# Kernel tuning notes

Measured on AMD Instinct MI355X. Metric: run time of the kernel, lower is better.

The kernel has to match this reference:

```python
import jax, jax.numpy as jnp
import numpy as np

S = 512      # seq_len -> S*S - S edges
V = 32000    # vocab_size
D = 128      # d_model
H = 4        # num_heads
L = 2        # num_layers
DN = 64      # d_node
DE = 64      # d_edge
DF = 4 * D   # ffn hidden
TEMP = 1.0   # temperature_init
E = S * S - S


def setup_inputs() -> dict:
    key = jax.random.key(0)
    ks = jax.random.split(key, 12)
    n = lambda k, shp: jax.random.normal(k, shp, dtype=jnp.float32) * 0.02
    return {
        "token_ids": jax.random.randint(ks[0], (S,), 0, V),
        "u": jax.random.uniform(ks[1], (E,), dtype=jnp.float32),
        "emb": n(ks[2], (V, D)),
        "Wqkv": n(ks[3], (L, D, 3 * D)), "bqkv": jnp.zeros((L, 3 * D)),
        "Wo": n(ks[4], (L, D, D)), "bo": jnp.zeros((L, D)),
        "ln1_g": jnp.ones((L, D)), "ln1_b": jnp.zeros((L, D)),
        "Wff1": n(ks[5], (L, D, DF)), "bff1": jnp.zeros((L, DF)),
        "Wff2": n(ks[6], (L, DF, D)), "bff2": jnp.zeros((L, D)),
        "ln2_g": jnp.ones((L, D)), "ln2_b": jnp.zeros((L, D)),
        "node_W": n(ks[7], (D, DN)), "node_b": jnp.zeros((DN,)),
        "sc_W1": n(ks[8], (2 * D + 1, D)), "sc_b1": jnp.zeros((D,)),
        "sc_W2": n(ks[9], (D, 1)), "sc_b2": jnp.zeros((1,)),
        "te_W": n(ks[10], (2 * D + 1, DE)), "te_b": jnp.zeros((DE,)),
    }


def _layernorm(x, g, b):
    m = jnp.mean(x, -1, keepdims=True)
    v = jnp.var(x, -1, keepdims=True)
    return (x - m) * jax.lax.rsqrt(v + 1e-5) * g + b


def _pos_encoding(s, d):
    pos = jnp.arange(s, dtype=jnp.float32)[:, None]
    div = jnp.exp(jnp.arange(0, d, 2, dtype=jnp.float32) * (-np.log(10000.0) / d))
    pe = jnp.zeros((s, d), dtype=jnp.float32)
    pe = pe.at[:, 0::2].set(jnp.sin(pos * div)).at[:, 1::2].set(jnp.cos(pos * div))
    return pe


_SRC_NP = np.repeat(np.arange(S), S)
_TGT_NP = np.tile(np.arange(S), S)
_KEEP = _SRC_NP != _TGT_NP
SRC = jnp.asarray(_SRC_NP[_KEEP])  # [E] static off-diagonal indices
TGT = jnp.asarray(_TGT_NP[_KEEP])


def _forward(token_ids, u, emb, Wqkv, bqkv, Wo, bo, ln1_g, ln1_b, Wff1, bff1,
             Wff2, bff2, ln2_g, ln2_b, node_W, node_b, sc_W1, sc_b1, sc_W2,
             sc_b2, te_W, te_b):
    # --- mini transformer backbone ---
    x = emb[token_ids] + _pos_encoding(S, D)  # [S, D]
    dh = D // H
    for l in range(L):
        qkv = x @ Wqkv[l] + bqkv[l]
        q, k, v = jnp.split(qkv, 3, axis=-1)
        q = q.reshape(S, H, dh); k = k.reshape(S, H, dh); v = v.reshape(S, H, dh)
        scores = jnp.einsum('qhd,khd->hqk', q, k) / np.sqrt(dh).astype(np.float32)
        attn = jax.nn.softmax(scores, axis=-1)
        o = jnp.einsum('hqk,khd->qhd', attn, v).reshape(S, D)
        x = _layernorm(x + o @ Wo[l] + bo[l], ln1_g[l], ln1_b[l])
        h = jax.nn.gelu(x @ Wff1[l] + bff1[l], approximate=False)
        x = _layernorm(x + h @ Wff2[l] + bff2[l], ln2_g[l], ln2_b[l])
    node_features = x @ node_W + node_b  # [S, DN]
    # --- all-pairs edge construction (off-diagonal) ---
    pos_diff = ((SRC - TGT).astype(jnp.float32) / S)[:, None]  # [E, 1]
    pair = jnp.concatenate([x[SRC], x[TGT], pos_diff], axis=-1)  # [E, 2D+1]
    # edge scorer MLP
    hs = jax.nn.gelu(pair @ sc_W1 + sc_b1, approximate=False)
    edge_logits = (hs @ sc_W2 + sc_b2)[:, 0]  # [E]
    # gumbel-sigmoid (soft, hard=False)
    uu = jnp.clip(u, 1e-8, 1.0 - 1e-8)
    gnoise = -jnp.log(-jnp.log(uu))
    edge_gates = jax.nn.sigmoid((edge_logits + gnoise) / TEMP)  # [E]
    # gated edge features
    edge_feats = (pair @ te_W + te_b) * edge_gates[:, None]  # [E, DE]
    return node_features, edge_feats, edge_gates


def reference(token_ids, u, emb, Wqkv, bqkv, Wo, bo, ln1_g, ln1_b, Wff1, bff1,
              Wff2, bff2, ln2_g, ln2_b, node_W, node_b, sc_W1, sc_b1, sc_W2,
              sc_b2, te_W, te_b):
    node_features, edge_feats, edge_gates = _forward(
        token_ids, u, emb, Wqkv, bqkv, Wo, bo, ln1_g, ln1_b, Wff1, bff1,
        Wff2, bff2, ln2_g, ln2_b, node_W, node_b, sc_W1, sc_b1, sc_W2,
        sc_b2, te_W, te_b)
    edge_index = jnp.stack([SRC, TGT])  # [2, E]
    return node_features, edge_feats, edge_index, edge_gates
```

## Files before the change

### kernel.cpp

```cpp
#include <hip/hip_runtime.h>
#include <math.h>

#define SS 512
#define DD 128
#define HH 4
#define DHH 32
#define DFF 512
#define E_EDGES 261632

__device__ __forceinline__ float gelu_f(float v) {
    return 0.5f * v * (1.0f + erff(v * 0.70710678118654752f));
}
__device__ __forceinline__ float fgelu(float x) {
    float x2 = x * x;
    float z = x * fmaf(-0.0713548164f, x2, -1.5957691216f);
    float e = __expf(z);
    return x * __builtin_amdgcn_rcpf(1.0f + e);
}

__global__ __launch_bounds__(256) void k_pre(const float* __restrict__ u,
                                             float* __restrict__ nl,
                                             float* __restrict__ out_ei,
                                             const int* __restrict__ tok,
                                             const float* __restrict__ emb,
                                             float* __restrict__ x) {
    int b = blockIdx.x;
    if (b < 1022) {
        int e = b * 256 + threadIdx.x;
        if (e >= E_EDGES) return;
        int s = e / 511;
        int idx = e - s * 511;
        int t = idx + (idx >= s);
        out_ei[e] = (float)s;
        out_ei[E_EDGES + e] = (float)t;
        float uu = fminf(fmaxf(u[e], 1e-8f), 1.0f - 1e-8f);
        nl[e] = -__logf(uu);
    } else {
        int i = (b - 1022) * 256 + threadIdx.x;
        int s = i >> 7, d = i & 127;
        float v = emb[(size_t)tok[s] * DD + d];
        int i2 = (d >> 1) << 1;
        float div = expf(-(float)i2 * (9.210340371976184f / 128.0f));
        float arg = (float)s * div;
        v += (d & 1) ? cosf(arg) : sinf(arg);
        x[i] = v;
    }
}

__global__ __launch_bounds__(384) void k_qkv(const float* __restrict__ x,
                                             const float* __restrict__ W,
                                             const float* __restrict__ b,
                                             float* __restrict__ qkv) {
    __shared__ float xs[2][DD];
    int r0 = blockIdx.x * 2;
    int c = threadIdx.x;
    if (c < 256) xs[c >> 7][c & 127] = x[r0 * DD + c];
    __syncthreads();
    float a0 = 0, a1 = 0;
    for (int d = 0; d < DD; ++d) {
        float w = W[d * 384 + c];
        a0 += xs[0][d] * w; a1 += xs[1][d] * w;
    }
    float bb = b[c];
    qkv[(r0 + 0) * 384 + c] = a0 + bb;
    qkv[(r0 + 1) * 384 + c] = a1 + bb;
}

__global__ __launch_bounds__(256) void k_attn(const float* __restrict__ qkv,
                                              float* __restrict__ o) {
    int q0 = blockIdx.x * 2, q1 = q0 + 1;
    int tid = threadIdx.x;
    int h = tid >> 6, lane = tid & 63;
    __shared__ float sq[2][DD];
    __shared__ float ps[2][HH][SS];
    __shared__ float tile[64 * 129];
    if (tid < 128) {
        sq[0][tid] = qkv[q0 * 384 + tid];
        sq[1][tid] = qkv[q1 * 384 + tid];
    }
    const float scale = 0.17677669529663687f;
    float sc0[8], sc1[8];
    float m0 = -1e30f, m1 = -1e30f;
    for (int kk = 0; kk < 8; ++kk) {
        __syncthreads();
        for (int i = tid * 4; i < 64 * 128; i += 1024) {
            int r = i >> 7, c = i & 127;
            const float4 v = *reinterpret_cast<const float4*>(&qkv[(kk * 64 + r) * 384 + 128 + c]);
            tile[r * 129 + c + 0] = v.x;
            tile[r * 129 + c + 1] = v.y;
            tile[r * 129 + c + 2] = v.z;
            tile[r * 129 + c + 3] = v.w;
        }
        __syncthreads();
        float a0 = 0.f, a1 = 0.f;
        #pragma unroll
        for (int d = 0; d < DHH; ++d) {
            float kv = tile[lane * 129 + h * DHH + d];
            a0 += sq[0][h * DHH + d] * kv;
            a1 += sq[1][h * DHH + d] * kv;
        }
        sc0[kk] = a0 * scale; sc1[kk] = a1 * scale;
        m0 = fmaxf(m0, sc0[kk]); m1 = fmaxf(m1, sc1[kk]);
    }
    for (int off = 32; off; off >>= 1) {
        m0 = fmaxf(m0, __shfl_xor(m0, off));
        m1 = fmaxf(m1, __shfl_xor(m1, off));
    }
    float s0 = 0.f, s1 = 0.f;
    for (int kk = 0; kk < 8; ++kk) {
        sc0[kk] = __expf(sc0[kk] - m0); s0 += sc0[kk];
        sc1[kk] = __expf(sc1[kk] - m1); s1 += sc1[kk];
    }
    for (int off = 32; off; off >>= 1) {
        s0 += __shfl_xor(s0, off);
        s1 += __shfl_xor(s1, off);
    }
    float i0 = 1.0f / s0, i1 = 1.0f / s1;
    for (int kk = 0; kk < 8; ++kk) {
        ps[0][h][kk * 64 + lane] = sc0[kk] * i0;
        ps[1][h][kk * 64 + lane] = sc1[kk] * i1;
    }
    __syncthreads();
    int d = lane & 31, hh2 = lane >> 5;
    float a0 = 0.f, a1 = 0.f;
    for (int i = 0; i < 256; ++i) {
        int ki = hh2 * 256 + i;
        float v = qkv[ki * 384 + 256 + h * DHH + d];
        a0 += ps[0][h][ki] * v;
        a1 += ps[1][h][ki] * v;
    }
    a0 += __shfl_down(a0, 32);
    a1 += __shfl_down(a1, 32);
    if (lane < 32) {
        o[q0 * DD + h * DHH + d] = a0;
        o[q1 * DD + h * DHH + d] = a1;
    }
}

__global__ __launch_bounds__(256) void k_tail(const float* __restrict__ o,
                                              const float* __restrict__ Wo,
                                              const float* __restrict__ bo,
                                              const float* __restrict__ g1,
                                              const float* __restrict__ b1,
                                              const float* __restrict__ W1,
                                              const float* __restrict__ bf1,
                                              const float* __restrict__ W2,
                                              const float* __restrict__ bf2,
                                              const float* __restrict__ g2,
                                              const float* __restrict__ b2,
                                              float* __restrict__ x) {
    int r0 = blockIdx.x * 2;
    int tid = threadIdx.x;
    int grp = tid >> 7, c = tid & 127;
    int wig = (tid >> 6) & 1;
    __shared__ float osr[2][DD];
    __shared__ float x1[2][DD];
    __shared__ float hh[2][DFF];
    __shared__ float red[2][2];
    osr[grp][c] = o[(r0 + grp) * DD + c];
    float xres = x[(r0 + grp) * DD + c];
    __syncthreads();
    float acc = 0.f;
    for (int d = 0; d < DD; ++d) acc += osr[grp][d] * Wo[d * DD + c];
    float val = xres + acc + bo[c];
    float sum = val;
    for (int off = 32; off; off >>= 1) sum += __shfl_xor(sum, off);
    if ((tid & 63) == 0) red[grp][wig] = sum;
    __syncthreads();
    float mean = (red[grp][0] + red[grp][1]) * (1.0f / 128.0f);
    float dv = val - mean;
    float sq = dv * dv;
    for (int off = 32; off; off >>= 1) sq += __shfl_xor(sq, off);
    __syncthreads();
    if ((tid & 63) == 0) red[grp][wig] = sq;
    __syncthreads();
    float var = (red[grp][0] + red[grp][1]) * (1.0f / 128.0f);
    float xv = dv * rsqrtf(var + 1e-5f) * g1[c] + b1[c];
    x1[grp][c] = xv;
    __syncthreads();
    {
        int c0 = tid, c1 = tid + 256;
        float s00 = 0, s01 = 0, s10 = 0, s11 = 0;
        for (int d = 0; d < DD; ++d) {
            float xa = x1[0][d], xb = x1[1][d];
            float w0 = W1[d * DFF + c0], w1 = W1[d * DFF + c1];
            s00 = fmaf(xa, w0, s00); s10 = fmaf(xb, w0, s10);
            s01 = fmaf(xa, w1, s01); s11 = fmaf(xb, w1, s11);
        }
        hh[0][c0] = gelu_f(s00 + bf1[c0]);
        hh[1][c0] = gelu_f(s10 + bf1[c0]);
        hh[0][c1] = gelu_f(s01 + bf1[c1]);
        hh[1][c1] = gelu_f(s11 + bf1[c1]);
    }
    __syncthreads();
    float acc2 = 0.f;
    for (int d = 0; d < DFF; ++d) acc2 += hh[grp][d] * W2[d * DD + c];
    float val2 = x1[grp][c] + acc2 + bf2[c];
    float sum2 = val2;
    for (int off = 32; off; off >>= 1) sum2 += __shfl_xor(sum2, off);
    if ((tid & 63) == 0) red[grp][wig] = sum2;
    __syncthreads();
    float mean2 = (red[grp][0] + red[grp][1]) * (1.0f / 128.0f);
    float dv2 = val2 - mean2;
    float sq2 = dv2 * dv2;
    for (int off = 32; off; off >>= 1) sq2 += __shfl_xor(sq2, off);
    __syncthreads();
    if ((tid & 63) == 0) red[grp][wig] = sq2;
    __syncthreads();
    float var2 = (red[grp][0] + red[grp][1]) * (1.0f / 128.0f);
    x[(r0 + grp) * DD + c] = dv2 * rsqrtf(var2 + 1e-5f) * g2[c] + b2[c];
}

__global__ __launch_bounds__(448) void k_node_pre(const float* __restrict__ x,
                                                  const float* __restrict__ nodeW,
                                                  const float* __restrict__ nodeb,
                                                  const float* __restrict__ scW1,
                                                  const float* __restrict__ scb1,
                                                  const float* __restrict__ teW,
                                                  const float* __restrict__ teb,
                                                  float* __restrict__ out_node,
                                                  float* __restrict__ As,
                                                  float* __restrict__ Atp,
                                                  float* __restrict__ Bs,
                                                  float* __restrict__ Btp) {
    __shared__ float xs[4][DD];
    int r0 = blockIdx.x * 4;
    for (int i = threadIdx.x; i < 4 * DD; i += 448)
        xs[i >> 7][i & 127] = x[(r0 + (i >> 7)) * DD + (i & 127)];
    __syncthreads();
    int c = threadIdx.x;
    const float* wp;
    int ldw;
    if (c < 64)       { wp = nodeW + c;                    ldw = 64;  }
    else if (c < 192) { wp = scW1 + (c - 64);              ldw = 128; }
    else if (c < 320) { wp = scW1 + 128 * 128 + (c - 192); ldw = 128; }
    else if (c < 384) { wp = teW + (c - 320);              ldw = 64;  }
    else              { wp = teW + 128 * 64 + (c - 384);   ldw = 64;  }
    float a[4] = {0, 0, 0, 0};
    for (int d = 0; d < DD; ++d) {
        float w = wp[d * ldw];
        a[0] += xs[0][d] * w; a[1] += xs[1][d] * w;
        a[2] += xs[2][d] * w; a[3] += xs[3][d] * w;
    }
    #pragma unroll
    for (int r = 0; r < 4; ++r) {
        int row = r0 + r;
        float v = a[r];
        if (c < 64)       out_node[row * 64 + c] = v + nodeb[c];
        else if (c < 192) As[row * 128 + (c - 64)] = v + scb1[c - 64];
        else if (c < 320) {
            int j0 = c - 192;
            int hhi = j0 >> 6, rem = j0 & 63;
            int jj = rem & 15, k = rem >> 4;
            Atp[row * 128 + jj * 8 + k * 2 + hhi] = v;
        }
        else if (c < 384) Bs[row * 64 + (c - 320)] = v + teb[c - 320];
        else {
            int jf = c - 384;
            int jj = jf & 15, k = jf >> 4;
            Btp[row * 64 + jj * 4 + k] = v;
        }
    }
}

__global__ __launch_bounds__(256) void k_edges(const float* __restrict__ As,
                                               const float* __restrict__ Atp,
                                               const float* __restrict__ Bs,
                                               const float* __restrict__ Btp,
                                               const float* __restrict__ scW1,
                                               const float* __restrict__ scW2,
                                               const float* __restrict__ scb2p,
                                               const float* __restrict__ teW,
                                               const float* __restrict__ nl,
                                               float* __restrict__ out_feat,
                                               float* __restrict__ out_gate) {
    int s = blockIdx.x;
    int seg = blockIdx.y;
    __shared__ float lAs[128], lap[128], lw2[128], lBs[64], lbp[64];
    int tid = threadIdx.x;
    if (tid < 128) {
        lAs[tid] = As[s * 128 + tid];
        lap[tid] = scW1[256 * 128 + tid];
        lw2[tid] = scW2[tid];
    } else if (tid < 192) {
        int j = tid - 128;
        lBs[j] = Bs[s * 64 + j];
        lbp[j] = teW[256 * 64 + j];
    }
    __syncthreads();
    int w = tid >> 6, lane = tid & 63;
    int g = lane >> 4, jj = lane & 15;
    float rAs[8], rap[8], rw2[8], rBs[4], rbp[4];
    #pragma unroll
    for (int k = 0; k < 4; ++k) {
        int j = jj + 16 * k;
        rAs[2 * k] = lAs[j]; rAs[2 * k + 1] = lAs[j + 64];
        rap[2 * k] = lap[j]; rap[2 * k + 1] = lap[j + 64];
        rw2[2 * k] = lw2[j]; rw2[2 * k + 1] = lw2[j + 64];
        rBs[k] = lBs[j]; rbp[k] = lbp[j];
    }
    float scb2 = scb2p[0];
    for (int iter = 0; iter < 16; ++iter) {
        int idx = seg * 256 + w * 64 + iter * 4 + g;
        if (idx >= 511) continue;
        int t = idx + (idx >= s);
        int e = s * 511 + idx;
        float pd = (float)(s - t) * (1.0f / 512.0f);
        const float4* ap = reinterpret_cast<const float4*>(&Atp[(size_t)t * 128 + jj * 8]);
        float4 at0 = ap[0];
        float4 at1 = ap[1];
        float part;
        float a;
        a = fmaf(pd, rap[0], rAs[0] + at0.x); part  = fgelu(a) * rw2[0];
        a = fmaf(pd, rap[1], rAs[1] + at0.y); part += fgelu(a) * rw2[1];
        a = fmaf(pd, rap[2], rAs[2] + at0.z); part += fgelu(a) * rw2[2];
        a = fmaf(pd, rap[3], rAs[3] + at0.w); part += fgelu(a) * rw2[3];
        a = fmaf(pd, rap[4], rAs[4] + at1.x); part += fgelu(a) * rw2[4];
        a = fmaf(pd, rap[5], rAs[5] + at1.y); part += fgelu(a) * rw2[5];
        a = fmaf(pd, rap[6], rAs[6] + at1.z); part += fgelu(a) * rw2[6];
        a = fmaf(pd, rap[7], rAs[7] + at1.w); part += fgelu(a) * rw2[7];
        part += __shfl_xor(part, 1);
        part += __shfl_xor(part, 2);
        part += __shfl_xor(part, 4);
        part += __shfl_xor(part, 8);
        float logit = part + scb2;
        float gate = __builtin_amdgcn_rcpf(1.0f + nl[e] * __expf(-logit));
        float4 bt = *reinterpret_cast<const float4*>(&Btp[(size_t)t * 64 + jj * 4]);
        float f0 = fmaf(pd, rbp[0], rBs[0] + bt.x) * gate;
        float f1 = fmaf(pd, rbp[1], rBs[1] + bt.y) * gate;
        float f2 = fmaf(pd, rbp[2], rBs[2] + bt.z) * gate;
        float f3 = fmaf(pd, rbp[3], rBs[3] + bt.w) * gate;
        size_t base = (size_t)e * 64 + jj;
        out_feat[base + 0]  = f0;
        out_feat[base + 16] = f1;
        out_feat[base + 32] = f2;
        out_feat[base + 48] = f3;
        if (jj == 0) out_gate[e] = gate;
    }
}

extern "C" void kernel_launch(void* const* d_in, const int* in_sizes, int n_in,
                              void* d_out, int out_size, void* d_ws, size_t ws_size,
                              hipStream_t stream) {
    const int*   tok   = (const int*)d_in[0];
    const float* u     = (const float*)d_in[1];
    const float* emb   = (const float*)d_in[2];
    const float* Wqkv  = (const float*)d_in[3];
    const float* bqkv  = (const float*)d_in[4];
    const float* Wo    = (const float*)d_in[5];
    const float* bo    = (const float*)d_in[6];
    const float* ln1g  = (const float*)d_in[7];
    const float* ln1b  = (const float*)d_in[8];
    const float* Wff1  = (const float*)d_in[9];
    const float* bff1  = (const float*)d_in[10];
    const float* Wff2  = (const float*)d_in[11];
    const float* bff2  = (const float*)d_in[12];
    const float* ln2g  = (const float*)d_in[13];
    const float* ln2b  = (const float*)d_in[14];
    const float* nodeW = (const float*)d_in[15];
    const float* nodeb = (const float*)d_in[16];
    const float* scW1  = (const float*)d_in[17];
    const float* scb1  = (const float*)d_in[18];
    const float* scW2  = (const float*)d_in[19];
    const float* scb2  = (const float*)d_in[20];
    const float* teW   = (const float*)d_in[21];
    const float* teb   = (const float*)d_in[22];

    float* out      = (float*)d_out;
    float* out_node = out;
    float* out_feat = out + 512 * 64;
    float* out_ei   = out_feat + (size_t)E_EDGES * 64;
    float* out_gate = out_ei + 2 * (size_t)E_EDGES;

    float* ws   = (float*)d_ws;
    float* x    = ws;
    float* qkv  = x + 512 * 128;
    float* o    = qkv + 512 * 384;
    float* As   = o + 512 * 128;
    float* Atp  = As + 512 * 128;
    float* Bs   = Atp + 512 * 128;
    float* Btp  = Bs + 512 * 64;
    float* nl   = Btp + 512 * 64;

    k_pre<<<dim3(1278), dim3(256), 0, stream>>>(u, nl, out_ei, tok, emb, x);
    for (int l = 0; l < 2; ++l) {
        k_qkv<<<dim3(256), dim3(384), 0, stream>>>(x, Wqkv + l * 128 * 384, bqkv + l * 384, qkv);
        k_attn<<<dim3(256), dim3(256), 0, stream>>>(qkv, o);
        k_tail<<<dim3(256), dim3(256), 0, stream>>>(o, Wo + l * 128 * 128, bo + l * 128,
                                                    ln1g + l * 128, ln1b + l * 128,
                                                    Wff1 + l * 128 * 512, bff1 + l * 512,
                                                    Wff2 + l * 512 * 128, bff2 + l * 128,
                                                    ln2g + l * 128, ln2b + l * 128, x);
    }
    k_node_pre<<<dim3(128), dim3(448), 0, stream>>>(x, nodeW, nodeb, scW1, scb1, teW, teb,
                                                    out_node, As, Atp, Bs, Btp);
    k_edges<<<dim3(512, 2), dim3(256), 0, stream>>>(As, Atp, Bs, Btp, scW1, scW2, scb2, teW, nl,
                                                    out_feat, out_gate);
}
```

Measured before the change: 277.7 us.

## Fuse kernels: embed into QKV, attention with tail and node projection, prep into edges

Folds the embedding and positional encoding into the first QKV kernel, and merges attention, output projection, FFN and layernorms into one kernel. In the last layer that kernel also does the node and edge-prep projections, and the -log(u) and edge_index writes move into the edge kernel. This cuts the launch count from 9 to 5 and drops the intermediate buffers o and nl. The P·V product now reads V through shared-memory tiles. The cost is a larger fused kernel with more shared memory, which may lower occupancy, and the node projection now runs in only 256 blocks.

After: 283.1 us. Within noise of the previous version (+2.0%).

```diff
diff --git a/kernel.cpp b/kernel.cpp
--- a/kernel.cpp
+++ b/kernel.cpp
@@ -18,43 +18,31 @@
     return x * __builtin_amdgcn_rcpf(1.0f + e);
 }
 
-__global__ __launch_bounds__(256) void k_pre(const float* __restrict__ u,
-                                             float* __restrict__ nl,
-                                             float* __restrict__ out_ei,
+template<int DO_EMBED>
+__global__ __launch_bounds__(384) void k_qkv(const float* __restrict__ xin,
                                              const int* __restrict__ tok,
                                              const float* __restrict__ emb,
-                                             float* __restrict__ x) {
-    int b = blockIdx.x;
-    if (b < 1022) {
-        int e = b * 256 + threadIdx.x;
-        if (e >= E_EDGES) return;
-        int s = e / 511;
-        int idx = e - s * 511;
-        int t = idx + (idx >= s);
-        out_ei[e] = (float)s;
-        out_ei[E_EDGES + e] = (float)t;
-        float uu = fminf(fmaxf(u[e], 1e-8f), 1.0f - 1e-8f);
-        nl[e] = -__logf(uu);
-    } else {
-        int i = (b - 1022) * 256 + threadIdx.x;
-        int s = i >> 7, d = i & 127;
-        float v = emb[(size_t)tok[s] * DD + d];
-        int i2 = (d >> 1) << 1;
-        float div = expf(-(float)i2 * (9.210340371976184f / 128.0f));
-        float arg = (float)s * div;
-        v += (d & 1) ? cosf(arg) : sinf(arg);
-        x[i] = v;
-    }
-}
-
-__global__ __launch_bounds__(384) void k_qkv(const float* __restrict__ x,
+                                             float* __restrict__ xout,
                                              const float* __restrict__ W,
                                              const float* __restrict__ b,
                                              float* __restrict__ qkv) {
     __shared__ float xs[2][DD];
     int r0 = blockIdx.x * 2;
     int c = threadIdx.x;
-    if (c < 256) xs[c >> 7][c & 127] = x[r0 * DD + c];
+    if (DO_EMBED) {
+        if (c < 256) {
+            int row = r0 + (c >> 7), d = c & 127;
+            float v = emb[(size_t)tok[row] * DD + d];
+            int i2 = (d >> 1) << 1;
+            float div = expf(-(float)i2 * (9.210340371976184f / 128.0f));
+            float arg = (float)row * div;
+            v += (d & 1) ? cosf(arg) : sinf(arg);
+            xs[c >> 7][d] = v;
+            xout[row * DD + d] = v;
+        }
+    } else {
+        if (c < 256) xs[c >> 7][c & 127] = xin[r0 * DD + c];
+    }
     __syncthreads();
     float a0 = 0, a1 = 0;
     for (int d = 0; d < DD; ++d) {
@@ -66,14 +54,42 @@
     qkv[(r0 + 1) * 384 + c] = a1 + bb;
 }
 
-__global__ __launch_bounds__(256) void k_attn(const float* __restrict__ qkv,
-                                              float* __restrict__ o) {
-    int q0 = blockIdx.x * 2, q1 = q0 + 1;
+template<int DO_NODE>
+__global__ __launch_bounds__(256) void k_attn_tail(const float* __restrict__ qkv,
+                                                   float* __restrict__ x,
+                                                   const float* __restrict__ Wo,
+                                                   const float* __restrict__ bo,
+                                                   const float* __restrict__ g1,
+                                                   const float* __restrict__ b1,
+                                                   const float* __restrict__ W1,
+                                                   const float* __restrict__ bf1,
+                                                   const float* __restrict__ W2,
+                                                   const float* __restrict__ bf2,
+                                                   const float* __restrict__ g2,
+                                                   const float* __restrict__ b2,
+                                                   const float* __restrict__ nodeW,
+                                                   const float* __restrict__ nodeb,
+                                                   const float* __restrict__ scW1,
+                                                   const float* __restrict__ scb1,
+                                                   const float* __restrict__ teW,
+                                                   const float* __restrict__ teb,
+                                                   float* __restrict__ out_node,
+                                                   float* __restrict__ As,
+                                                   float* __restrict__ Atp,
+                                                   float* __restrict__ Bs,
+                                                   float* __restrict__ Btp) {
+    int r0 = blockIdx.x * 2;
+    int q0 = r0, q1 = r0 + 1;
     int tid = threadIdx.x;
     int h = tid >> 6, lane = tid & 63;
     __shared__ float sq[2][DD];
     __shared__ float ps[2][HH][SS];
     __shared__ float tile[64 * 129];
+    __shared__ float os[2][DD];
+    __shared__ float x1[2][DD];
+    __shared__ float hh[2][DFF];
+    __shared__ float xf[2][DD];
+    __shared__ float red[2][2];
     if (tid < 128) {
         sq[0][tid] = qkv[q0 * 384 + tid];
         sq[1][tid] = qkv[q1 * 384 + tid];
@@ -120,59 +136,49 @@
         ps[0][h][kk * 64 + lane] = sc0[kk] * i0;
         ps[1][h][kk * 64 + lane] = sc1[kk] * i1;
     }
-    __syncthreads();
     int d = lane & 31, hh2 = lane >> 5;
     float a0 = 0.f, a1 = 0.f;
-    for (int i = 0; i < 256; ++i) {
-        int ki = hh2 * 256 + i;
-        float v = qkv[ki * 384 + 256 + h * DHH + d];
-        a0 += ps[0][h][ki] * v;
-        a1 += ps[1][h][ki] * v;
+    for (int kk = 0; kk < 8; ++kk) {
+        __syncthreads();
+        for (int i = tid * 4; i < 64 * 128; i += 1024) {
+            int r = i >> 7, c = i & 127;
+            const float4 v = *reinterpret_cast<const float4*>(&qkv[(kk * 64 + r) * 384 + 256 + c]);
+            tile[r * 129 + c + 0] = v.x;
+            tile[r * 129 + c + 1] = v.y;
+            tile[r * 129 + c + 2] = v.z;
+            tile[r * 129 + c + 3] = v.w;
+        }
+        __syncthreads();
+        #pragma unroll
+        for (int i = 0; i < 32; ++i) {
+            int key = hh2 * 32 + i;
+            float v = tile[key * 129 + h * DHH + d];
+            a0 += ps[0][h][kk * 64 + key] * v;
+            a1 += ps[1][h][kk * 64 + key] * v;
+        }
     }
     a0 += __shfl_down(a0, 32);
     a1 += __shfl_down(a1, 32);
     if (lane < 32) {
-        o[q0 * DD + h * DHH + d] = a0;
-        o[q1 * DD + h * DHH + d] = a1;
-    }
-}
-
-__global__ __launch_bounds__(256) void k_tail(const float* __restrict__ o,
-                                              const float* __restrict__ Wo,
-                                              const float* __restrict__ bo,
-                                              const float* __restrict__ g1,
-                                              const float* __restrict__ b1,
-                                              const float* __restrict__ W1,
-                                              const float* __restrict__ bf1,
-                                              const float* __restrict__ W2,
-                                              const float* __restrict__ bf2,
-                                              const float* __restrict__ g2,
-                                              const float* __restrict__ b2,
-                                              float* __restrict__ x) {
-    int r0 = blockIdx.x * 2;
-    int tid = threadIdx.x;
+        os[0][h * DHH + d] = a0;
+        os[1][h * DHH + d] = a1;
+    }
+    __syncthreads();
     int grp = tid >> 7, c = tid & 127;
     int wig = (tid >> 6) & 1;
-    __shared__ float osr[2][DD];
-    __shared__ float x1[2][DD];
-    __shared__ float hh[2][DFF];
-    __shared__ float red[2][2];
-    osr[grp][c] = o[(r0 + grp) * DD + c];
-    float xres = x[(r0 + grp) * DD + c];
-    __syncthreads();
     float acc = 0.f;
-    for (int d = 0; d < DD; ++d) acc += osr[grp][d] * Wo[d * DD + c];
-    float val = xres + acc + bo[c];
+    for (int dd = 0; dd < DD; ++dd) acc += os[grp][dd] * Wo[dd * DD + c];
+    float val = x[(r0 + grp) * DD + c] + acc + bo[c];
     float sum = val;
     for (int off = 32; off; off >>= 1) sum += __shfl_xor(sum, off);
     if ((tid & 63) == 0) red[grp][wig] = sum;
     __syncthreads();
     float mean = (red[grp][0] + red[grp][1]) * (1.0f / 128.0f);
     float dv = val - mean;
-    float sq = dv * dv;
-    for (int off = 32; off; off >>= 1) sq += __shfl_xor(sq, off);
-    __syncthreads();
-    if ((tid & 63) == 0) red[grp][wig] = sq;
+    float sqv = dv * dv;
+    for (int off = 32; off; off >>= 1) sqv += __shfl_xor(sqv, off);
+    __syncthreads();
+    if ((tid & 63) == 0) red[grp][wig] = sqv;
     __syncthreads();
     float var = (red[grp][0] + red[grp][1]) * (1.0f / 128.0f);
     float xv = dv * rsqrtf(var + 1e-5f) * g1[c] + b1[c];
@@ -181,9 +187,9 @@
     {
         int c0 = tid, c1 = tid + 256;
         float s00 = 0, s01 = 0, s10 = 0, s11 = 0;
-        for (int d = 0; d < DD; ++d) {
-            float xa = x1[0][d], xb = x1[1][d];
-            float w0 = W1[d * DFF + c0], w1 = W1[d * DFF + c1];
+        for (int dd = 0; dd < DD; ++dd) {
+            float xa = x1[0][dd], xb = x1[1][dd];
+            float w0 = W1[dd * DFF + c0], w1 = W1[dd * DFF + c1];
             s00 = fmaf(xa, w0, s00); s10 = fmaf(xb, w0, s10);
             s01 = fmaf(xa, w1, s01); s11 = fmaf(xb, w1, s11);
         }
@@ -194,7 +200,7 @@
     }
     __syncthreads();
     float acc2 = 0.f;
-    for (int d = 0; d < DFF; ++d) acc2 += hh[grp][d] * W2[d * DD + c];
+    for (int dd = 0; dd < DFF; ++dd) acc2 += hh[grp][dd] * W2[dd * DD + c];
     float val2 = x1[grp][c] + acc2 + bf2[c];
     float sum2 = val2;
     for (int off = 32; off; off >>= 1) sum2 += __shfl_xor(sum2, off);
@@ -208,57 +214,36 @@
     if ((tid & 63) == 0) red[grp][wig] = sq2;
     __syncthreads();
     float var2 = (red[grp][0] + red[grp][1]) * (1.0f / 128.0f);
-    x[(r0 + grp) * DD + c] = dv2 * rsqrtf(var2 + 1e-5f) * g2[c] + b2[c];
-}
-
-__global__ __launch_bounds__(448) void k_node_pre(const float* __restrict__ x,
-                                                  const float* __restrict__ nodeW,
-                                                  const float* __restrict__ nodeb,
-                                                  const float* __restrict__ scW1,
-                                                  const float* __restrict__ scb1,
-                                                  const float* __restrict__ teW,
-                                                  const float* __restrict__ teb,
-                                                  float* __restrict__ out_node,
-                                                  float* __restrict__ As,
-                                                  float* __restrict__ Atp,
-                                                  float* __restrict__ Bs,
-                                                  float* __restrict__ Btp) {
-    __shared__ float xs[4][DD];
-    int r0 = blockIdx.x * 4;
-    for (int i = threadIdx.x; i < 4 * DD; i += 448)
-        xs[i >> 7][i & 127] = x[(r0 + (i >> 7)) * DD + (i & 127)];
-    __syncthreads();
-    int c = threadIdx.x;
-    const float* wp;
-    int ldw;
-    if (c < 64)       { wp = nodeW + c;                    ldw = 64;  }
-    else if (c < 192) { wp = scW1 + (c - 64);              ldw = 128; }
-    else if (c < 320) { wp = scW1 + 128 * 128 + (c - 192); ldw = 128; }
-    else if (c < 384) { wp = teW + (c - 320);              ldw = 64;  }
-    else              { wp = teW + 128 * 64 + (c - 384);   ldw = 64;  }
-    float a[4] = {0, 0, 0, 0};
-    for (int d = 0; d < DD; ++d) {
-        float w = wp[d * ldw];
-        a[0] += xs[0][d] * w; a[1] += xs[1][d] * w;
-        a[2] += xs[2][d] * w; a[3] += xs[3][d] * w;
-    }
-    #pragma unroll
-    for (int r = 0; r < 4; ++r) {
-        int row = r0 + r;
-        float v = a[r];
-        if (c < 64)       out_node[row * 64 + c] = v + nodeb[c];
-        else if (c < 192) As[row * 128 + (c - 64)] = v + scb1[c - 64];
-        else if (c < 320) {
-            int j0 = c - 192;
-            int hhi = j0 >> 6, rem = j0 & 63;
-            int jj = rem & 15, k = rem >> 4;
-            Atp[row * 128 + jj * 8 + k * 2 + hhi] = v;
-        }
-        else if (c < 384) Bs[row * 64 + (c - 320)] = v + teb[c - 320];
+    float outv = dv2 * rsqrtf(var2 + 1e-5f) * g2[c] + b2[c];
+    if (!DO_NODE) {
+        x[(r0 + grp) * DD + c] = outv;
+        return;
+    }
+    xf[grp][c] = outv;
+    __syncthreads();
+    for (int c0 = tid; c0 < 896; c0 += 256) {
+        int rl = (c0 >= 448) ? 1 : 0;
+        int cc = c0 - rl * 448;
+        int row = r0 + rl;
+        const float* wp; int ldw; float bias = 0.f;
+        if (cc < 64)       { wp = nodeW + cc;                     ldw = 64;  bias = nodeb[cc]; }
+        else if (cc < 192) { wp = scW1 + (cc - 64);               ldw = 128; bias = scb1[cc - 64]; }
+        else if (cc < 320) { wp = scW1 + 128 * 128 + (cc - 192);  ldw = 128; }
+        else if (cc < 384) { wp = teW + (cc - 320);               ldw = 64;  bias = teb[cc - 320]; }
+        else               { wp = teW + 128 * 64 + (cc - 384);    ldw = 64;  }
+        float a = bias;
+        for (int dd = 0; dd < DD; ++dd) a += xf[rl][dd] * wp[dd * ldw];
+        if (cc < 64)       out_node[row * 64 + cc] = a;
+        else if (cc < 192) As[row * 128 + (cc - 64)] = a;
+        else if (cc < 320) {
+            int j0 = cc - 192;
+            int hhi = j0 >> 6, rem = j0 & 63, jj = rem & 15, k = rem >> 4;
+            Atp[row * 128 + jj * 8 + k * 2 + hhi] = a;
+        }
+        else if (cc < 384) Bs[row * 64 + (cc - 320)] = a;
         else {
-            int jf = c - 384;
-            int jj = jf & 15, k = jf >> 4;
-            Btp[row * 64 + jj * 4 + k] = v;
+            int jf = cc - 384, jj = jf & 15, k = jf >> 4;
+            Btp[row * 64 + jj * 4 + k] = a;
         }
     }
 }
@@ -271,9 +256,10 @@
                                                const float* __restrict__ scW2,
                                                const float* __restrict__ scb2p,
                                                const float* __restrict__ teW,
-                                               const float* __restrict__ nl,
+                                               const float* __restrict__ u,
                                                float* __restrict__ out_feat,
-                                               float* __restrict__ out_gate) {
+                                               float* __restrict__ out_gate,
+                                               float* __restrict__ out_ei) {
     int s = blockIdx.x;
     int seg = blockIdx.y;
     __shared__ float lAs[128], lap[128], lw2[128], lBs[64], lbp[64];
@@ -309,8 +295,7 @@
         const float4* ap = reinterpret_cast<const float4*>(&Atp[(size_t)t * 128 + jj * 8]);
         float4 at0 = ap[0];
         float4 at1 = ap[1];
-        float part;
-        float a;
+        float part, a;
         a = fmaf(pd, rap[0], rAs[0] + at0.x); part  = fgelu(a) * rw2[0];
         a = fmaf(pd, rap[1], rAs[1] + at0.y); part += fgelu(a) * rw2[1];
         a = fmaf(pd, rap[2], rAs[2] + at0.z); part += fgelu(a) * rw2[2];
@@ -324,7 +309,9 @@
         part += __shfl_xor(part, 4);
         part += __shfl_xor(part, 8);
         float logit = part + scb2;
-        float gate = __builtin_amdgcn_rcpf(1.0f + nl[e] * __expf(-logit));
+        float uu = fminf(fmaxf(u[e], 1e-8f), 1.0f - 1e-8f);
+        float nlv = -__logf(uu);
+        float gate = __builtin_amdgcn_rcpf(1.0f + nlv * __expf(-logit));
         float4 bt = *reinterpret_cast<const float4*>(&Btp[(size_t)t * 64 + jj * 4]);
         float f0 = fmaf(pd, rbp[0], rBs[0] + bt.x) * gate;
         float f1 = fmaf(pd, rbp[1], rBs[1] + bt.y) * gate;
@@ -335,7 +322,8 @@
         out_feat[base + 16] = f1;
         out_feat[base + 32] = f2;
         out_feat[base + 48] = f3;
-        if (jj == 0) out_gate[e] = gate;
+        if (jj == 0) { out_gate[e] = gate; out_ei[e] = (float)s; }
+        else if (jj == 1) out_ei[E_EDGES + e] = (float)t;
     }
 }
 
@@ -375,25 +363,28 @@
     float* ws   = (float*)d_ws;
     float* x    = ws;
     float* qkv  = x + 512 * 128;
-    float* o    = qkv + 512 * 384;
-    float* As   = o + 512 * 128;
+    float* As   = qkv + 512 * 384;
     float* Atp  = As + 512 * 128;
     float* Bs   = Atp + 512 * 128;
     float* Btp  = Bs + 512 * 64;
-    float* nl   = Btp + 512 * 64;
-
-    k_pre<<<dim3(1278), dim3(256), 0, stream>>>(u, nl, out_ei, tok, emb, x);
-    for (int l = 0; l < 2; ++l) {
-        k_qkv<<<dim3(256), dim3(384), 0, stream>>>(x, Wqkv + l * 128 * 384, bqkv + l * 384, qkv);
-        k_attn<<<dim3(256), dim3(256), 0, stream>>>(qkv, o);
-        k_tail<<<dim3(256), dim3(256), 0, stream>>>(o, Wo + l * 128 * 128, bo + l * 128,
-                                                    ln1g + l * 128, ln1b + l * 128,
-                                                    Wff1 + l * 128 * 512, bff1 + l * 512,
-                                                    Wff2 + l * 512 * 128, bff2 + l * 128,
-                                                    ln2g + l * 128, ln2b + l * 128, x);
-    }
-    k_node_pre<<<dim3(128), dim3(448), 0, stream>>>(x, nodeW, nodeb, scW1, scb1, teW, teb,
-                                                    out_node, As, Atp, Bs, Btp);
-    k_edges<<<dim3(512, 2), dim3(256), 0, stream>>>(As, Atp, Bs, Btp, scW1, scW2, scb2, teW, nl,
-                                                    out_feat, out_gate);
-}
+
+    k_qkv<1><<<dim3(256), dim3(384), 0, stream>>>(nullptr, tok, emb, x,
+                                                  Wqkv, bqkv, qkv);
+    k_attn_tail<0><<<dim3(256), dim3(256), 0, stream>>>(qkv, x, Wo, bo,
+                                                        ln1g, ln1b, Wff1, bff1, Wff2, bff2,
+                                                        ln2g, ln2b,
+                                                        nullptr, nullptr, nullptr, nullptr,
+                                                        nullptr, nullptr,
+                                                        nullptr, nullptr, nullptr, nullptr, nullptr);
+    k_qkv<0><<<dim3(256), dim3(384), 0, stream>>>(x, nullptr, nullptr, nullptr,
+                                                  Wqkv + 128 * 384, bqkv + 384, qkv);
+    k_attn_tail<1><<<dim3(256), dim3(256), 0, stream>>>(qkv, x, Wo + 128 * 128, bo + 128,
+                                                        ln1g + 128, ln1b + 128,
+                                                        Wff1 + 128 * 512, bff1 + 512,
+                                                        Wff2 + 512 * 128, bff2 + 128,
+                                                        ln2g + 128, ln2b + 128,
+                                                        nodeW, nodeb, scW1, scb1, teW, teb,
+                                                        out_node, As, Atp, Bs, Btp);
+    k_edges<<<dim3(512, 2), dim3(256), 0, stream>>>(As, Atp, Bs, Btp, scW1, scW2, scb2, teW, u,
+                                                    out_feat, out_gate, out_ei);
+}
```
